# Performance work log

Measured on AMD Instinct MI355X. Metric: run time of the kernel, lower is better.

The kernel has to match this reference:

```python
import jax, jax.numpy as jnp
import numpy as np

D_MODEL = 1024
N_HEADS = 16
D_K = D_MODEL // N_HEADS
B, S = 2, 2048


def setup_inputs() -> dict:
    key = jax.random.key(0)
    ks = jax.random.split(key, 11)
    def lin(kw, kb, fan_in):
        bound = 1.0 / np.sqrt(fan_in)
        W = jax.random.uniform(kw, (fan_in, D_MODEL), jnp.float32, -bound, bound)
        b = jax.random.uniform(kb, (D_MODEL,), jnp.float32, -bound, bound)
        return W, b
    Wq, bq = lin(ks[0], ks[1], D_MODEL)
    Wk, bk = lin(ks[2], ks[3], D_MODEL)
    Wv, bv = lin(ks[4], ks[5], D_MODEL)
    Wo, bo = lin(ks[6], ks[7], D_MODEL)
    q = jax.random.normal(ks[8], (B, S, D_MODEL), jnp.float32)
    k = jax.random.normal(ks[9], (B, S, D_MODEL), jnp.float32)
    v = jax.random.normal(ks[10], (B, S, D_MODEL), jnp.float32)
    return {"q": q, "k": k, "v": v,
            "Wq": Wq, "bq": bq, "Wk": Wk, "bk": bk,
            "Wv": Wv, "bv": bv, "Wo": Wo, "bo": bo}


def reference(q, k, v, Wq, bq, Wk, bk, Wv, bv, Wo, bo):
    Bz, Sq, _ = q.shape
    def split_heads(x):  # [B,S,D] -> [B,H,S,d_k]
        return x.reshape(x.shape[0], x.shape[1], N_HEADS, D_K).transpose(0, 2, 1, 3)
    qh = split_heads(q @ Wq + bq)
    kh = split_heads(k @ Wk + bk)
    vh = split_heads(v @ Wv + bv)
    scores = jnp.einsum("bhqd,bhkd->bhqk", qh, kh) / jnp.sqrt(jnp.float32(D_K))
    attn = jax.nn.softmax(scores, axis=-1)
    out = jnp.einsum("bhqk,bhkd->bhqd", attn, vh)
    out = out.transpose(0, 2, 1, 3).reshape(Bz, Sq, D_MODEL)
    return out @ Wo + bo
```

## Files before the change

### kernel.cpp

```cpp
#include <hip/hip_runtime.h>
#include <hip/hip_bf16.h>
#include <stdint.h>

typedef __bf16 bf16;
typedef __bf16 bf16x8 __attribute__((ext_vector_type(8)));
typedef __bf16 bf16x4 __attribute__((ext_vector_type(4)));
typedef float  f32x4  __attribute__((ext_vector_type(4)));
typedef float  f32x16 __attribute__((ext_vector_type(16)));
typedef uint32_t u32;

#define MFMA16(a,b,c) __builtin_amdgcn_mfma_f32_16x16x32_bf16((a),(b),(c),0,0,0)
#define MFMA32(a,b,c) __builtin_amdgcn_mfma_f32_32x32x16_bf16((a),(b),(c),0,0,0)

#define QSCL 0.1803368801111204f

__device__ __forceinline__ u32 sx32(u32 x) {
    return (u32)__shfl_xor((int)x, 32, 64);
}
__device__ __forceinline__ float swapred_max(float v) {
    return fmaxf(v, __builtin_bit_cast(float, sx32(__builtin_bit_cast(u32, v))));
}
__device__ __forceinline__ float swapred_sum(float v) {
    return v + __builtin_bit_cast(float, sx32(__builtin_bit_cast(u32, v)));
}
__device__ __forceinline__ u32 pkbf(float lo, float hi) {
    union { bf16 h[2]; u32 u; } un;
    un.h[0] = (bf16)lo; un.h[1] = (bf16)hi;
    return un.u;
}
__device__ __forceinline__ void pack_frags(const float* p, int hi, bf16x8& f0, bf16x8& f1) {
    u32 k01 = pkbf(p[0],  p[1]),  k23 = pkbf(p[2],  p[3]);
    u32 k45 = pkbf(p[4],  p[5]),  k67 = pkbf(p[6],  p[7]);
    u32 k89 = pkbf(p[8],  p[9]),  kab = pkbf(p[10], p[11]);
    u32 kcd = pkbf(p[12], p[13]), kef = pkbf(p[14], p[15]);
    u32 x01 = sx32(k01), x23 = sx32(k23), x45 = sx32(k45), x67 = sx32(k67);
    u32 x89 = sx32(k89), xab = sx32(kab), xcd = sx32(kcd), xef = sx32(kef);
    union { u32 w[4]; bf16x8 v; } u0, u1;
    u0.w[0] = hi ? x45 : k01;  u0.w[1] = hi ? x67 : k23;
    u0.w[2] = hi ? k45 : x01;  u0.w[3] = hi ? k67 : x23;
    u1.w[0] = hi ? xcd : k89;  u1.w[1] = hi ? xef : kab;
    u1.w[2] = hi ? kcd : x89;  u1.w[3] = hi ? kef : xab;
    f0 = u0.v; f1 = u1.v;
}

__global__ __launch_bounds__(256) void k_cvt3(const float* __restrict__ a, const float* __restrict__ b,
                                              const float* __restrict__ c,
                                              bf16* __restrict__ x, bf16* __restrict__ y,
                                              bf16* __restrict__ z) {
    int i = blockIdx.x * 256 + threadIdx.x;
    int t = i >> 20;
    int r = (i & 1048575) << 2;
    const float* s = (t == 0) ? a : ((t == 1) ? b : c);
    bf16* d = (t == 0) ? x : ((t == 1) ? y : z);
    float4 v = *(const float4*)&s[r];
    bf16x4 w = {(bf16)v.x, (bf16)v.y, (bf16)v.z, (bf16)v.w};
    *(bf16x4*)&d[r] = w;
}
__global__ __launch_bounds__(256) void k_cvt1(const float* __restrict__ s, bf16* __restrict__ d) {
    int r = (blockIdx.x * 256 + threadIdx.x) << 2;
    float4 v = *(const float4*)&s[r];
    bf16x4 w = {(bf16)v.x, (bf16)v.y, (bf16)v.z, (bf16)v.w};
    *(bf16x4*)&d[r] = w;
}

__global__ __launch_bounds__(256) void k_transpose_w(const float* __restrict__ W,
                                                     bf16* __restrict__ Wt, float scale) {
    __shared__ bf16 t[64][65];
    const int n0 = blockIdx.x * 64, k0 = blockIdx.y * 64;
    for (int i = 0; i < 16; ++i) {
        int idx = threadIdx.x + i * 256, r = idx >> 6, c = idx & 63;
        t[r][c] = (bf16)(W[(size_t)(k0 + r) * 1024 + n0 + c] * scale);
    }
    __syncthreads();
    for (int i = 0; i < 16; ++i) {
        int idx = threadIdx.x + i * 256, r = idx >> 6, c = idx & 63;
        Wt[(size_t)(n0 + r) * 1024 + k0 + c] = t[c][r];
    }
}

__device__ __forceinline__ void gemm_tile(const bf16* __restrict__ A, const bf16* __restrict__ Bt,
                                          const float* __restrict__ bias, float bscale,
                                          void* __restrict__ Cp, int out_mode, int m0, int n0,
                                          bf16 (*As)[64], bf16 (*Bs)[64]) {
    const int tid = threadIdx.x;
    const int wid = tid >> 6, lane = tid & 63, lg = lane >> 4, lm = lane & 15;
    const int wr = wid >> 1, wc = wid & 1;
    const int grow = tid >> 3, gcol = (tid & 7) << 3;

    f32x4 acc[4][4] = {};

    for (int kt = 0; kt < 16; ++kt) {
        const int k0 = kt << 6;
        __syncthreads();
#pragma unroll
        for (int p = 0; p < 4; ++p) {
            __builtin_amdgcn_global_load_lds(
                (const __attribute__((address_space(1))) void*)(A + (size_t)(m0 + p * 32 + grow) * 1024 + k0 + gcol),
                (__attribute__((address_space(3))) void*)(&As[p * 32 + wid * 8][0]), 16, 0, 0);
            __builtin_amdgcn_global_load_lds(
                (const __attribute__((address_space(1))) void*)(Bt + (size_t)(n0 + p * 32 + grow) * 1024 + k0 + gcol),
                (__attribute__((address_space(3))) void*)(&Bs[p * 32 + wid * 8][0]), 16, 0, 0);
        }
        __syncthreads();
#pragma unroll
        for (int kk = 0; kk < 2; ++kk) {
            bf16x8 a[4], b[4];
#pragma unroll
            for (int i = 0; i < 4; ++i) a[i] = *(const bf16x8*)&As[wr * 64 + i * 16 + lm][kk * 32 + lg * 8];
#pragma unroll
            for (int j = 0; j < 4; ++j) b[j] = *(const bf16x8*)&Bs[wc * 64 + j * 16 + lm][kk * 32 + lg * 8];
#pragma unroll
            for (int i = 0; i < 4; ++i)
#pragma unroll
                for (int j = 0; j < 4; ++j) acc[i][j] = MFMA16(a[i], b[j], acc[i][j]);
        }
    }

    for (int i = 0; i < 4; ++i) {
        for (int j = 0; j < 4; ++j) {
            int col = n0 + wc * 64 + j * 16 + lm;
            for (int q = 0; q < 4; ++q) {
                int row = m0 + wr * 64 + i * 16 + lg * 4 + q;
                if (out_mode == 0) {
                    float val = acc[i][j][q] + bscale * bias[col];
                    int bb = row >> 11, s = row & 2047, h = col >> 6, d = col & 63;
                    ((bf16*)Cp)[(((size_t)bb * 16 + h) * 2048 + s) * 64 + d] = (bf16)val;
                } else {
                    float val = acc[i][j][q] + bias[row];
                    size_t idx = (((size_t)(col >> 11) * 16 + (row >> 6)) * 64 + (row & 63)) * 2048 + (col & 2047);
                    ((bf16*)Cp)[idx] = (bf16)val;
                }
            }
        }
    }
}

__device__ __forceinline__ void tile_decode(int r, int& m0, int& n0) {
    int xcd = r & 7, slot = (r >> 3) & 3, n = (r >> 5) & 7;
    m0 = (xcd * 4 + slot) * 128;
    n0 = n * 128;
}
__device__ __forceinline__ void tile_decode_vt(int r, int& m0, int& n0) {
    int xcd = r & 7, loc = r >> 3;
    int nslot = loc & 3, m = loc >> 2;
    n0 = (xcd * 4 + nslot) * 128;
    m0 = m * 128;
}

__global__ __launch_bounds__(256, 4) void k_gemm_proj(const bf16* __restrict__ A,
                                                      const bf16* __restrict__ Bt,
                                                      const float* __restrict__ bias, float bscale,
                                                      void* __restrict__ Cp) {
    __shared__ bf16 As[128][64];
    __shared__ bf16 Bs[128][64];
    int m0, n0;
    tile_decode(blockIdx.x, m0, n0);
    gemm_tile(A, Bt, bias, bscale, Cp, 0, m0, n0, As, Bs);
}

__global__ __launch_bounds__(256, 4) void k_gemm_vt(const bf16* __restrict__ Wtv,
                                                    const bf16* __restrict__ vc,
                                                    const float* __restrict__ bias,
                                                    bf16* __restrict__ Vtb) {
    __shared__ bf16 As[128][64];
    __shared__ bf16 Bs[128][64];
    int m0, n0;
    tile_decode_vt(blockIdx.x, m0, n0);
    gemm_tile(Wtv, vc, bias, 1.0f, (void*)Vtb, 2, m0, n0, As, Bs);
}

__global__ __launch_bounds__(256, 4) void k_gemm_qkv(const bf16* __restrict__ qc, const bf16* __restrict__ kc,
                                                     const bf16* __restrict__ vc,
                                                     const bf16* __restrict__ Wtq, const bf16* __restrict__ Wtk,
                                                     const bf16* __restrict__ Wtv,
                                                     const float* __restrict__ bq, const float* __restrict__ bk,
                                                     const float* __restrict__ bv,
                                                     bf16* __restrict__ Qb, bf16* __restrict__ Kb,
                                                     bf16* __restrict__ Vtb) {
    __shared__ bf16 As[128][64];
    __shared__ bf16 Bs[128][64];
    int l = blockIdx.x, z = l >> 8, r = l & 255;
    int m0, n0;
    if (z == 2) {
        tile_decode_vt(r, m0, n0);
        gemm_tile(Wtv, vc, bv, 1.0f, (void*)Vtb, 2, m0, n0, As, Bs);
    } else {
        tile_decode(r, m0, n0);
        const bf16* A  = (z == 0) ? qc : kc;
        const bf16* Bt = (z == 0) ? Wtq : Wtk;
        const float* bias = (z == 0) ? bq : bk;
        float bscale = (z == 0) ? QSCL : 1.0f;
        bf16* Cp = (z == 0) ? Qb : Kb;
        gemm_tile(A, Bt, bias, bscale, (void*)Cp, 0, m0, n0, As, Bs);
    }
}

__global__ __launch_bounds__(256, 4) void k_gemm_out(const bf16* __restrict__ A,
                                                     const bf16* __restrict__ Bt,
                                                     const float* __restrict__ bias,
                                                     float* __restrict__ C) {
    __shared__ bf16 As[128][64];
    __shared__ bf16 Bs[64][64];
    const int tid = threadIdx.x;
    const int wid = tid >> 6, lane = tid & 63, lg = lane >> 4, lm = lane & 15;
    const int grow = tid >> 3, gcol = (tid & 7) << 3;
    const int r = blockIdx.x;
    const int xcd = r & 7, loc = r >> 3;
    const int mslot = loc & 3, n = loc >> 2;
    const int m0 = (xcd * 4 + mslot) * 128, n0 = n * 64;

    f32x4 acc[2][4] = {};

    for (int kt = 0; kt < 16; ++kt) {
        const int k0 = kt << 6;
        __syncthreads();
#pragma unroll
        for (int p = 0; p < 4; ++p)
            __builtin_amdgcn_global_load_lds(
                (const __attribute__((address_space(1))) void*)(A + (size_t)(m0 + p * 32 + grow) * 1024 + k0 + gcol),
                (__attribute__((address_space(3))) void*)(&As[p * 32 + wid * 8][0]), 16, 0, 0);
#pragma unroll
        for (int p = 0; p < 2; ++p)
            __builtin_amdgcn_global_load_lds(
                (const __attribute__((address_space(1))) void*)(Bt + (size_t)(n0 + p * 32 + grow) * 1024 + k0 + gcol),
                (__attribute__((address_space(3))) void*)(&Bs[p * 32 + wid * 8][0]), 16, 0, 0);
        __syncthreads();
#pragma unroll
        for (int kk = 0; kk < 2; ++kk) {
            bf16x8 a[2], b[4];
#pragma unroll
            for (int i = 0; i < 2; ++i) a[i] = *(const bf16x8*)&As[wid * 32 + i * 16 + lm][kk * 32 + lg * 8];
#pragma unroll
            for (int j = 0; j < 4; ++j) b[j] = *(const bf16x8*)&Bs[j * 16 + lm][kk * 32 + lg * 8];
#pragma unroll
            for (int i = 0; i < 2; ++i)
#pragma unroll
                for (int j = 0; j < 4; ++j) acc[i][j] = MFMA16(a[i], b[j], acc[i][j]);
        }
    }

    for (int i = 0; i < 2; ++i) {
        for (int j = 0; j < 4; ++j) {
            int col = n0 + j * 16 + lm;
            float bv = bias[col];
            for (int q = 0; q < 4; ++q) {
                int row = m0 + wid * 32 + i * 16 + lg * 4 + q;
                C[(size_t)row * 1024 + col] = acc[i][j][q] + bv;
            }
        }
    }
}

__global__ __launch_bounds__(512, 2) void k_attn(const bf16* __restrict__ Q,
                                                 const bf16* __restrict__ Kb,
                                                 const bf16* __restrict__ Vt,
                                                 bf16* __restrict__ Out) {
    __shared__ bf16 Ks[2][64 * 64];
    __shared__ bf16 Vs[2][64 * 64];
    const int tid = threadIdx.x;
    const int wid = tid >> 6, lane = tid & 63;
    const int lm = lane & 31, hi = lane >> 5;
    const int bid = blockIdx.x;
    const int bh = bid & 31, qt = bid >> 5;
    const int bb = bh >> 4, h = bh & 15;
    const int qrow = qt * 256 + wid * 32 + lm;
    const size_t qk_base = (size_t)bh * (2048 * 64);
    const size_t vt_base = (size_t)bh * (64 * 2048);

    const int srow = tid >> 3, sc8 = tid & 7;
    const int cse = (sc8 ^ (srow & 7)) * 8;
    const bf16* kstage = Kb + qk_base + (size_t)srow * 64 + cse;
    const bf16* vstage = Vt + vt_base + (size_t)srow * 2048 + cse;
    const int ldsoff = wid * 1024;

    bf16x8 qf[4];
    {
        const bf16* qp = Q + qk_base + (size_t)qrow * 64 + hi * 8;
#pragma unroll
        for (int f = 0; f < 4; ++f) qf[f] = *(const bf16x8*)(qp + f * 16);
    }

    f32x16 O0 = {}, O1 = {};
    float mrow = -1e30f, lsum = 0.f;

    const int swz = (lm & 7);

    __builtin_amdgcn_global_load_lds(
        (const __attribute__((address_space(1))) void*)(kstage),
        (__attribute__((address_space(3))) void*)((char*)&Ks[0][0] + ldsoff), 16, 0, 0);
    __builtin_amdgcn_global_load_lds(
        (const __attribute__((address_space(1))) void*)(vstage),
        (__attribute__((address_space(3))) void*)((char*)&Vs[0][0] + ldsoff), 16, 0, 0);
    __syncthreads();

    int cur = 0;
#pragma unroll 1
    for (int kt = 0; kt < 32; ++kt) {
        if (kt + 1 < 32) {
            __builtin_amdgcn_global_load_lds(
                (const __attribute__((address_space(1))) void*)(kstage + (size_t)(kt + 1) * 4096),
                (__attribute__((address_space(3))) void*)((char*)&Ks[cur ^ 1][0] + ldsoff), 16, 0, 0);
            __builtin_amdgcn_global_load_lds(
                (const __attribute__((address_space(1))) void*)(vstage + (size_t)(kt + 1) * 64),
                (__attribute__((address_space(3))) void*)((char*)&Vs[cur ^ 1][0] + ldsoff), 16, 0, 0);
        }

        const char* Ksc = (const char*)&Ks[cur][0];
        const char* Vsc = (const char*)&Vs[cur][0];

        bf16x8 kf0[4], kf1[4];
#pragma unroll
        for (int f = 0; f < 4; ++f) {
            int ch = (f << 1) | hi;
            kf0[f] = *(const bf16x8*)(Ksc + lm * 128 + ((ch ^ swz) << 4));
            kf1[f] = *(const bf16x8*)(Ksc + (lm + 32) * 128 + ((ch ^ swz) << 4));
        }
        bf16x8 vf0[4], vf1[4];
#pragma unroll
        for (int ks = 0; ks < 4; ++ks) {
            int ch = (ks << 1) | hi;
            vf0[ks] = *(const bf16x8*)(Vsc + lm * 128 + ((ch ^ swz) << 4));
            vf1[ks] = *(const bf16x8*)(Vsc + (lm + 32) * 128 + ((ch ^ swz) << 4));
        }

        f32x16 s0 = {}, s1 = {};
#pragma unroll
        for (int f = 0; f < 4; ++f) {
            s0 = MFMA32(kf0[f], qf[f], s0);
            s1 = MFMA32(kf1[f], qf[f], s1);
        }

        float pe0[16], pe1[16];
#pragma unroll
        for (int r = 0; r < 16; ++r) pe0[r] = __builtin_amdgcn_exp2f(s0[r] - mrow);
#pragma unroll
        for (int r = 0; r < 16; ++r) pe1[r] = __builtin_amdgcn_exp2f(s1[r] - mrow);

        float t8[8];
#pragma unroll
        for (int r = 0; r < 8; ++r)
            t8[r] = fmaxf(fmaxf(s0[r], s0[r + 8]), fmaxf(s1[r], s1[r + 8]));
#pragma unroll
        for (int st = 4; st; st >>= 1)
#pragma unroll
            for (int r = 0; r < st; ++r) t8[r] = fmaxf(t8[r], t8[r + st]);
        float pm = swapred_max(t8[0]);

        if (!__all(pm <= mrow + 8.0f)) {
            float mnew = fmaxf(mrow, pm);
            float corr = __builtin_amdgcn_exp2f(mrow - mnew);
            lsum *= corr;
            O0 *= corr;
            O1 *= corr;
            mrow = mnew;
#pragma unroll
            for (int r = 0; r < 16; ++r) pe0[r] = __builtin_amdgcn_exp2f(s0[r] - mrow);
#pragma unroll
            for (int r = 0; r < 16; ++r) pe1[r] = __builtin_amdgcn_exp2f(s1[r] - mrow);
        }

        float u8[8];
#pragma unroll
        for (int r = 0; r < 8; ++r) u8[r] = (pe0[r] + pe0[r + 8]) + (pe1[r] + pe1[r + 8]);
#pragma unroll
        for (int st = 4; st; st >>= 1)
#pragma unroll
            for (int r = 0; r < st; ++r) u8[r] = u8[r] + u8[r + st];
        lsum += u8[0];

        bf16x8 pf[4];
        pack_frags(pe0, hi, pf[0], pf[1]);
        pack_frags(pe1, hi, pf[2], pf[3]);

#pragma unroll
        for (int ks = 0; ks < 4; ++ks) {
            O0 = MFMA32(vf0[ks], pf[ks], O0);
            O1 = MFMA32(vf1[ks], pf[ks], O1);
        }

        __syncthreads();
        cur ^= 1;
    }

    float lrow = swapred_sum(lsum);
    float inv = 1.0f / lrow;
    bf16* op = Out + ((size_t)bb * 2048 + qrow) * 1024 + h * 64 + 4 * hi;
#pragma unroll
    for (int t = 0; t < 4; ++t) {
        bf16x4 w0, w1;
#pragma unroll
        for (int e = 0; e < 4; ++e) {
            w0[e] = (bf16)(O0[4 * t + e] * inv);
            w1[e] = (bf16)(O1[4 * t + e] * inv);
        }
        *(bf16x4*)(op + 8 * t)      = w0;
        *(bf16x4*)(op + 32 + 8 * t) = w1;
    }
}

extern "C" void kernel_launch(void* const* d_in, const int* in_sizes, int n_in,
                              void* d_out, int out_size, void* d_ws, size_t ws_size,
                              hipStream_t stream) {
    const float* q  = (const float*)d_in[0];
    const float* k  = (const float*)d_in[1];
    const float* v  = (const float*)d_in[2];
    const float* Wq = (const float*)d_in[3];
    const float* bq = (const float*)d_in[4];
    const float* Wk = (const float*)d_in[5];
    const float* bk = (const float*)d_in[6];
    const float* Wv = (const float*)d_in[7];
    const float* bv = (const float*)d_in[8];
    const float* Wo = (const float*)d_in[9];
    const float* bo = (const float*)d_in[10];

    char* ws = (char*)d_ws;
    const size_t MB = 1ull << 20;
    const dim3 twg(16, 16), blk(256);

    if (ws_size >= 64 * MB) {
        bf16* Wtq = (bf16*)(ws + 0 * MB);
        bf16* Wtk = (bf16*)(ws + 2 * MB);
        bf16* Wtv = (bf16*)(ws + 4 * MB);
        bf16* Wto = (bf16*)(ws + 6 * MB);
        bf16* qc  = (bf16*)(ws + 8 * MB);
        bf16* kc  = (bf16*)(ws + 16 * MB);
        bf16* vc  = (bf16*)(ws + 24 * MB);
        bf16* Qb  = (bf16*)(ws + 32 * MB);
        bf16* Kb  = (bf16*)(ws + 40 * MB);
        bf16* Vtb = (bf16*)(ws + 48 * MB);
        bf16* AOb = kc;

        k_transpose_w<<<twg, blk, 0, stream>>>(Wq, Wtq, QSCL);
        k_transpose_w<<<twg, blk, 0, stream>>>(Wk, Wtk, 1.0f);
        k_transpose_w<<<twg, blk, 0, stream>>>(Wv, Wtv, 1.0f);
        k_transpose_w<<<twg, blk, 0, stream>>>(Wo, Wto, 1.0f);
        k_cvt3<<<12288, blk, 0, stream>>>(q, k, v, qc, kc, vc);
        k_gemm_qkv<<<768, blk, 0, stream>>>(qc, kc, vc, Wtq, Wtk, Wtv, bq, bk, bv, Qb, Kb, Vtb);
        k_attn<<<256, 512, 0, stream>>>(Qb, Kb, Vtb, AOb);
        k_gemm_out<<<512, blk, 0, stream>>>(AOb, Wto, bo, (float*)d_out);
    } else {
        bf16* Wt   = (bf16*)(ws + 0 * MB);
        bf16* Qb   = (bf16*)(ws + 2 * MB);
        bf16* Kb   = (bf16*)(ws + 10 * MB);
        bf16* Vtb  = (bf16*)(ws + 18 * MB);
        bf16* AOb  = (bf16*)(ws + 26 * MB);
        bf16* Cb   = (bf16*)d_out;

        k_cvt1<<<4096, blk, 0, stream>>>(q, Cb);
        k_transpose_w<<<twg, blk, 0, stream>>>(Wq, Wt, QSCL);
        k_gemm_proj<<<256, blk, 0, stream>>>(Cb, Wt, bq, QSCL, (void*)Qb);
        k_cvt1<<<4096, blk, 0, stream>>>(k, Cb);
        k_transpose_w<<<twg, blk, 0, stream>>>(Wk, Wt, 1.0f);
        k_gemm_proj<<<256, blk, 0, stream>>>(Cb, Wt, bk, 1.0f, (void*)Kb);
        k_cvt1<<<4096, blk, 0, stream>>>(v, Cb);
        k_transpose_w<<<twg, blk, 0, stream>>>(Wv, Wt, 1.0f);
        k_gemm_vt<<<256, blk, 0, stream>>>(Wt, Cb, bv, Vtb);
        k_transpose_w<<<twg, blk, 0, stream>>>(Wo, Wt, 1.0f);
        k_attn<<<256, 512, 0, stream>>>(Qb, Kb, Vtb, AOb);
        k_gemm_out<<<512, blk, 0, stream>>>(AOb, Wt, bo, (float*)d_out);
    }
}
```

Measured before the change: 144.2 us.

## Split attention over KV halves with a combine pass; merge weight transposes

The attention kernel now splits the key/value sequence into two halves per block, and each wave handles 64 query rows (two 32-row groups) against 32-key tiles. Unnormalized partial outputs go to a bf16 scratch buffer, with row max and sum stored separately. A new combine kernel merges the two partials into the head-interleaved layout. The four weight-transpose launches also become one launch over a z grid dimension. The aim is to reuse each K/V LDS tile for more query rows and cut launch overhead, at the cost of an extra kernel pass and extra global traffic for the partials.

```diff
diff --git a/kernel.cpp b/kernel.cpp
--- a/kernel.cpp
+++ b/kernel.cpp
@@ -63,10 +63,9 @@
     *(bf16x4*)&d[r] = w;
 }
 
-__global__ __launch_bounds__(256) void k_transpose_w(const float* __restrict__ W,
-                                                     bf16* __restrict__ Wt, float scale) {
+__device__ __forceinline__ void transpose_body(const float* __restrict__ W, bf16* __restrict__ Wt,
+                                               float scale, int n0, int k0) {
     __shared__ bf16 t[64][65];
-    const int n0 = blockIdx.x * 64, k0 = blockIdx.y * 64;
     for (int i = 0; i < 16; ++i) {
         int idx = threadIdx.x + i * 256, r = idx >> 6, c = idx & 63;
         t[r][c] = (bf16)(W[(size_t)(k0 + r) * 1024 + n0 + c] * scale);
@@ -76,6 +75,19 @@
         int idx = threadIdx.x + i * 256, r = idx >> 6, c = idx & 63;
         Wt[(size_t)(n0 + r) * 1024 + k0 + c] = t[c][r];
     }
+}
+__global__ __launch_bounds__(256) void k_transpose_w(const float* __restrict__ W,
+                                                     bf16* __restrict__ Wt, float scale) {
+    transpose_body(W, Wt, scale, blockIdx.x * 64, blockIdx.y * 64);
+}
+__global__ __launch_bounds__(256) void k_transpose_w4(const float* __restrict__ Wq, const float* __restrict__ Wk,
+                                                      const float* __restrict__ Wv, const float* __restrict__ Wo,
+                                                      bf16* __restrict__ Wtq, bf16* __restrict__ Wtk,
+                                                      bf16* __restrict__ Wtv, bf16* __restrict__ Wto) {
+    int z = blockIdx.z;
+    const float* W = (z == 0) ? Wq : (z == 1) ? Wk : (z == 2) ? Wv : Wo;
+    bf16* Wt = (z == 0) ? Wtq : (z == 1) ? Wtk : (z == 2) ? Wtv : Wto;
+    transpose_body(W, Wt, (z == 0) ? QSCL : 1.0f, blockIdx.x * 64, blockIdx.y * 64);
 }
 
 __device__ __forceinline__ void gemm_tile(const bf16* __restrict__ A, const bf16* __restrict__ Bt,
@@ -254,148 +266,187 @@
 __global__ __launch_bounds__(512, 2) void k_attn(const bf16* __restrict__ Q,
                                                  const bf16* __restrict__ Kb,
                                                  const bf16* __restrict__ Vt,
-                                                 bf16* __restrict__ Out) {
-    __shared__ bf16 Ks[2][64 * 64];
-    __shared__ bf16 Vs[2][64 * 64];
+                                                 bf16* __restrict__ Opart,
+                                                 float* __restrict__ ml) {
+    __shared__ bf16 Ks[2][32 * 64];
+    __shared__ bf16 Vs[2][32 * 64];
     const int tid = threadIdx.x;
     const int wid = tid >> 6, lane = tid & 63;
     const int lm = lane & 31, hi = lane >> 5;
     const int bid = blockIdx.x;
-    const int bh = bid & 31, qt = bid >> 5;
-    const int bb = bh >> 4, h = bh & 15;
-    const int qrow = qt * 256 + wid * 32 + lm;
+    const int bh = bid & 31, qt = (bid >> 5) & 3, sp = bid >> 7;
     const size_t qk_base = (size_t)bh * (2048 * 64);
     const size_t vt_base = (size_t)bh * (64 * 2048);
-
-    const int srow = tid >> 3, sc8 = tid & 7;
-    const int cse = (sc8 ^ (srow & 7)) * 8;
-    const bf16* kstage = Kb + qk_base + (size_t)srow * 64 + cse;
-    const bf16* vstage = Vt + vt_base + (size_t)srow * 2048 + cse;
-    const int ldsoff = wid * 1024;
-
-    bf16x8 qf[4];
+    const int kt0 = sp * 32, kt1 = kt0 + 32;
+    const int qrowA = qt * 512 + wid * 64 + lm;
+    const int qrowB = qrowA + 32;
+
+    const int u = tid & 255;
+    const int srow = u >> 3, pc = u & 7;
+    const int lc = pc ^ (srow & 7);
+    const bf16* kst = Kb + qk_base + (size_t)srow * 64 + lc * 8;
+    const bf16* vst = Vt + vt_base + (size_t)(srow + ((lc >> 2) << 5)) * 2048 + (lc & 3) * 8;
+    const int sbase = (wid & 3) * 1024;
+
+#define STAGE(T, BUF)                                                                             \
+    do {                                                                                          \
+        if (tid < 256)                                                                            \
+            __builtin_amdgcn_global_load_lds(                                                     \
+                (const __attribute__((address_space(1))) void*)(kst + (size_t)(T) * 2048),        \
+                (__attribute__((address_space(3))) void*)((char*)&Ks[BUF][0] + sbase), 16, 0, 0); \
+        else                                                                                      \
+            __builtin_amdgcn_global_load_lds(                                                     \
+                (const __attribute__((address_space(1))) void*)(vst + (size_t)(T) * 32),          \
+                (__attribute__((address_space(3))) void*)((char*)&Vs[BUF][0] + sbase), 16, 0, 0); \
+    } while (0)
+
+    bf16x8 qfA[4], qfB[4];
     {
-        const bf16* qp = Q + qk_base + (size_t)qrow * 64 + hi * 8;
-#pragma unroll
-        for (int f = 0; f < 4; ++f) qf[f] = *(const bf16x8*)(qp + f * 16);
-    }
-
-    f32x16 O0 = {}, O1 = {};
-    float mrow = -1e30f, lsum = 0.f;
-
-    const int swz = (lm & 7);
-
-    __builtin_amdgcn_global_load_lds(
-        (const __attribute__((address_space(1))) void*)(kstage),
-        (__attribute__((address_space(3))) void*)((char*)&Ks[0][0] + ldsoff), 16, 0, 0);
-    __builtin_amdgcn_global_load_lds(
-        (const __attribute__((address_space(1))) void*)(vstage),
-        (__attribute__((address_space(3))) void*)((char*)&Vs[0][0] + ldsoff), 16, 0, 0);
+        const bf16* qpA = Q + qk_base + (size_t)qrowA * 64 + hi * 8;
+        const bf16* qpB = qpA + 32 * 64;
+#pragma unroll
+        for (int f = 0; f < 4; ++f) {
+            qfA[f] = *(const bf16x8*)(qpA + f * 16);
+            qfB[f] = *(const bf16x8*)(qpB + f * 16);
+        }
+    }
+
+    f32x16 O0A = {}, O1A = {}, O0B = {}, O1B = {};
+    float mA = -1e30f, mB = -1e30f, lsA = 0.f, lsB = 0.f;
+    const int swz = lm & 7;
+
+    STAGE(kt0, 0);
     __syncthreads();
 
     int cur = 0;
 #pragma unroll 1
-    for (int kt = 0; kt < 32; ++kt) {
-        if (kt + 1 < 32) {
-            __builtin_amdgcn_global_load_lds(
-                (const __attribute__((address_space(1))) void*)(kstage + (size_t)(kt + 1) * 4096),
-                (__attribute__((address_space(3))) void*)((char*)&Ks[cur ^ 1][0] + ldsoff), 16, 0, 0);
-            __builtin_amdgcn_global_load_lds(
-                (const __attribute__((address_space(1))) void*)(vstage + (size_t)(kt + 1) * 64),
-                (__attribute__((address_space(3))) void*)((char*)&Vs[cur ^ 1][0] + ldsoff), 16, 0, 0);
-        }
+    for (int kt = kt0; kt < kt1; ++kt) {
+        if (kt + 1 < kt1) STAGE(kt + 1, cur ^ 1);
 
         const char* Ksc = (const char*)&Ks[cur][0];
         const char* Vsc = (const char*)&Vs[cur][0];
 
-        bf16x8 kf0[4], kf1[4];
-#pragma unroll
-        for (int f = 0; f < 4; ++f) {
-            int ch = (f << 1) | hi;
-            kf0[f] = *(const bf16x8*)(Ksc + lm * 128 + ((ch ^ swz) << 4));
-            kf1[f] = *(const bf16x8*)(Ksc + (lm + 32) * 128 + ((ch ^ swz) << 4));
-        }
-        bf16x8 vf0[4], vf1[4];
-#pragma unroll
-        for (int ks = 0; ks < 4; ++ks) {
-            int ch = (ks << 1) | hi;
-            vf0[ks] = *(const bf16x8*)(Vsc + lm * 128 + ((ch ^ swz) << 4));
-            vf1[ks] = *(const bf16x8*)(Vsc + (lm + 32) * 128 + ((ch ^ swz) << 4));
-        }
-
-        f32x16 s0 = {}, s1 = {};
-#pragma unroll
-        for (int f = 0; f < 4; ++f) {
-            s0 = MFMA32(kf0[f], qf[f], s0);
-            s1 = MFMA32(kf1[f], qf[f], s1);
-        }
-
-        float pe0[16], pe1[16];
-#pragma unroll
-        for (int r = 0; r < 16; ++r) pe0[r] = __builtin_amdgcn_exp2f(s0[r] - mrow);
-#pragma unroll
-        for (int r = 0; r < 16; ++r) pe1[r] = __builtin_amdgcn_exp2f(s1[r] - mrow);
-
-        float t8[8];
-#pragma unroll
-        for (int r = 0; r < 8; ++r)
-            t8[r] = fmaxf(fmaxf(s0[r], s0[r + 8]), fmaxf(s1[r], s1[r + 8]));
+        bf16x8 kf[4];
+#pragma unroll
+        for (int f = 0; f < 4; ++f)
+            kf[f] = *(const bf16x8*)(Ksc + lm * 128 + (((((f << 1) | hi)) ^ swz) << 4));
+
+        f32x16 sA = {}, sB = {};
+#pragma unroll
+        for (int f = 0; f < 4; ++f) sA = MFMA32(kf[f], qfA[f], sA);
+#pragma unroll
+        for (int f = 0; f < 4; ++f) sB = MFMA32(kf[f], qfB[f], sB);
+
+        float tA[8], tB[8];
+#pragma unroll
+        for (int r = 0; r < 8; ++r) { tA[r] = fmaxf(sA[r], sA[r + 8]); tB[r] = fmaxf(sB[r], sB[r + 8]); }
 #pragma unroll
         for (int st = 4; st; st >>= 1)
 #pragma unroll
-            for (int r = 0; r < st; ++r) t8[r] = fmaxf(t8[r], t8[r + st]);
-        float pm = swapred_max(t8[0]);
-
-        if (!__all(pm <= mrow + 8.0f)) {
-            float mnew = fmaxf(mrow, pm);
-            float corr = __builtin_amdgcn_exp2f(mrow - mnew);
-            lsum *= corr;
-            O0 *= corr;
-            O1 *= corr;
-            mrow = mnew;
-#pragma unroll
-            for (int r = 0; r < 16; ++r) pe0[r] = __builtin_amdgcn_exp2f(s0[r] - mrow);
-#pragma unroll
-            for (int r = 0; r < 16; ++r) pe1[r] = __builtin_amdgcn_exp2f(s1[r] - mrow);
-        }
-
-        float u8[8];
-#pragma unroll
-        for (int r = 0; r < 8; ++r) u8[r] = (pe0[r] + pe0[r + 8]) + (pe1[r] + pe1[r + 8]);
+            for (int r = 0; r < st; ++r) { tA[r] = fmaxf(tA[r], tA[r + st]); tB[r] = fmaxf(tB[r], tB[r + st]); }
+        float pmA = swapred_max(tA[0]);
+        float pmB = swapred_max(tB[0]);
+
+        if (!__all(pmA <= mA + 8.0f)) {
+            float mn = fmaxf(mA, pmA);
+            float c = __builtin_amdgcn_exp2f(mA - mn);
+            lsA *= c; O0A *= c; O1A *= c; mA = mn;
+        }
+        if (!__all(pmB <= mB + 8.0f)) {
+            float mn = fmaxf(mB, pmB);
+            float c = __builtin_amdgcn_exp2f(mB - mn);
+            lsB *= c; O0B *= c; O1B *= c; mB = mn;
+        }
+
+        float peA[16], peB[16];
+#pragma unroll
+        for (int r = 0; r < 16; ++r) peA[r] = __builtin_amdgcn_exp2f(sA[r] - mA);
+#pragma unroll
+        for (int r = 0; r < 16; ++r) peB[r] = __builtin_amdgcn_exp2f(sB[r] - mB);
+        float uA[8], uB[8];
+#pragma unroll
+        for (int r = 0; r < 8; ++r) { uA[r] = peA[r] + peA[r + 8]; uB[r] = peB[r] + peB[r + 8]; }
 #pragma unroll
         for (int st = 4; st; st >>= 1)
 #pragma unroll
-            for (int r = 0; r < st; ++r) u8[r] = u8[r] + u8[r + st];
-        lsum += u8[0];
-
-        bf16x8 pf[4];
-        pack_frags(pe0, hi, pf[0], pf[1]);
-        pack_frags(pe1, hi, pf[2], pf[3]);
-
-#pragma unroll
-        for (int ks = 0; ks < 4; ++ks) {
-            O0 = MFMA32(vf0[ks], pf[ks], O0);
-            O1 = MFMA32(vf1[ks], pf[ks], O1);
-        }
+            for (int r = 0; r < st; ++r) { uA[r] += uA[r + st]; uB[r] += uB[r + st]; }
+        lsA += uA[0];
+        lsB += uB[0];
+
+        bf16x8 pfA[2], pfB[2];
+        pack_frags(peA, hi, pfA[0], pfA[1]);
+        pack_frags(peB, hi, pfB[0], pfB[1]);
+
+        bf16x8 vf[2][2];
+#pragma unroll
+        for (int dh = 0; dh < 2; ++dh)
+#pragma unroll
+            for (int ks = 0; ks < 2; ++ks)
+                vf[dh][ks] = *(const bf16x8*)(Vsc + lm * 128 + ((((dh << 2) | (ks << 1) | hi) ^ swz) << 4));
+
+        O0A = MFMA32(vf[0][0], pfA[0], O0A);
+        O0A = MFMA32(vf[0][1], pfA[1], O0A);
+        O1A = MFMA32(vf[1][0], pfA[0], O1A);
+        O1A = MFMA32(vf[1][1], pfA[1], O1A);
+        O0B = MFMA32(vf[0][0], pfB[0], O0B);
+        O0B = MFMA32(vf[0][1], pfB[1], O0B);
+        O1B = MFMA32(vf[1][0], pfB[0], O1B);
+        O1B = MFMA32(vf[1][1], pfB[1], O1B);
 
         __syncthreads();
         cur ^= 1;
     }
-
-    float lrow = swapred_sum(lsum);
-    float inv = 1.0f / lrow;
-    bf16* op = Out + ((size_t)bb * 2048 + qrow) * 1024 + h * 64 + 4 * hi;
+#undef STAGE
+
+    float lrA = swapred_sum(lsA);
+    float lrB = swapred_sum(lsB);
+    const size_t r2A = ((size_t)bh * 2048 + qrowA) * 2 + sp;
+    const size_t r2B = r2A + 64;
+    bf16* opA = Opart + r2A * 64 + 4 * hi;
+    bf16* opB = Opart + r2B * 64 + 4 * hi;
 #pragma unroll
     for (int t = 0; t < 4; ++t) {
-        bf16x4 w0, w1;
+        bf16x4 a0, a1, b0, b1;
 #pragma unroll
         for (int e = 0; e < 4; ++e) {
-            w0[e] = (bf16)(O0[4 * t + e] * inv);
-            w1[e] = (bf16)(O1[4 * t + e] * inv);
-        }
-        *(bf16x4*)(op + 8 * t)      = w0;
-        *(bf16x4*)(op + 32 + 8 * t) = w1;
-    }
+            a0[e] = (bf16)O0A[4 * t + e];
+            a1[e] = (bf16)O1A[4 * t + e];
+            b0[e] = (bf16)O0B[4 * t + e];
+            b1[e] = (bf16)O1B[4 * t + e];
+        }
+        *(bf16x4*)(opA + 8 * t)      = a0;
+        *(bf16x4*)(opA + 32 + 8 * t) = a1;
+        *(bf16x4*)(opB + 8 * t)      = b0;
+        *(bf16x4*)(opB + 32 + 8 * t) = b1;
+    }
+    if (hi == 0) {
+        float2 vA = {mA, lrA};
+        float2 vB = {mB, lrB};
+        ((float2*)ml)[r2A] = vA;
+        ((float2*)ml)[r2B] = vB;
+    }
+}
+
+__global__ __launch_bounds__(256) void k_combine(const bf16* __restrict__ Opart,
+                                                 const float* __restrict__ ml,
+                                                 bf16* __restrict__ AOb) {
+    int e8 = blockIdx.x * 256 + threadIdx.x;
+    int row = e8 >> 3, dc = (e8 & 7) << 3;
+    float2 ml0 = ((const float2*)ml)[row * 2 + 0];
+    float2 ml1 = ((const float2*)ml)[row * 2 + 1];
+    float M  = fmaxf(ml0.x, ml1.x);
+    float w0 = __builtin_amdgcn_exp2f(ml0.x - M);
+    float w1 = __builtin_amdgcn_exp2f(ml1.x - M);
+    float L  = w0 * ml0.y + w1 * ml1.y;
+    float a0 = w0 / L, a1 = w1 / L;
+    bf16x8 p0 = *(const bf16x8*)&Opart[((size_t)row * 2 + 0) * 64 + dc];
+    bf16x8 p1 = *(const bf16x8*)&Opart[((size_t)row * 2 + 1) * 64 + dc];
+    bf16x8 o;
+#pragma unroll
+    for (int j = 0; j < 8; ++j) o[j] = (bf16)(a0 * (float)p0[j] + a1 * (float)p1[j]);
+    int bh = row >> 11, qrow = row & 2047;
+    int bb = bh >> 4, h = bh & 15;
+    *(bf16x8*)&AOb[((size_t)bb * 2048 + qrow) * 1024 + h * 64 + dc] = o;
 }
 
 extern "C" void kernel_launch(void* const* d_in, const int* in_sizes, int n_in,
@@ -416,6 +467,7 @@
     char* ws = (char*)d_ws;
     const size_t MB = 1ull << 20;
     const dim3 twg(16, 16), blk(256);
+    bf16* Opart = (bf16*)d_out;
 
     if (ws_size >= 64 * MB) {
         bf16* Wtq = (bf16*)(ws + 0 * MB);
@@ -428,23 +480,23 @@
         bf16* Qb  = (bf16*)(ws + 32 * MB);
         bf16* Kb  = (bf16*)(ws + 40 * MB);
         bf16* Vtb = (bf16*)(ws + 48 * MB);
-        bf16* AOb = kc;
-
-        k_transpose_w<<<twg, blk, 0, stream>>>(Wq, Wtq, QSCL);
-        k_transpose_w<<<twg, blk, 0, stream>>>(Wk, Wtk, 1.0f);
-        k_transpose_w<<<twg, blk, 0, stream>>>(Wv, Wtv, 1.0f);
-        k_transpose_w<<<twg, blk, 0, stream>>>(Wo, Wto, 1.0f);
+        float* mlb = (float*)qc;
+        bf16* AOb  = kc;
+
+        k_transpose_w4<<<dim3(16, 16, 4), blk, 0, stream>>>(Wq, Wk, Wv, Wo, Wtq, Wtk, Wtv, Wto);
         k_cvt3<<<12288, blk, 0, stream>>>(q, k, v, qc, kc, vc);
         k_gemm_qkv<<<768, blk, 0, stream>>>(qc, kc, vc, Wtq, Wtk, Wtv, bq, bk, bv, Qb, Kb, Vtb);
-        k_attn<<<256, 512, 0, stream>>>(Qb, Kb, Vtb, AOb);
+        k_attn<<<256, 512, 0, stream>>>(Qb, Kb, Vtb, Opart, mlb);
+        k_combine<<<2048, blk, 0, stream>>>(Opart, mlb, AOb);
         k_gemm_out<<<512, blk, 0, stream>>>(AOb, Wto, bo, (float*)d_out);
     } else {
         bf16* Wt   = (bf16*)(ws + 0 * MB);
         bf16* Qb   = (bf16*)(ws + 2 * MB);
         bf16* Kb   = (bf16*)(ws + 10 * MB);
         bf16* Vtb  = (bf16*)(ws + 18 * MB);
-        bf16* AOb  = (bf16*)(ws + 26 * MB);
+        float* mlb = (float*)(ws + 26 * MB);
         bf16* Cb   = (bf16*)d_out;
+        bf16* AOb  = Qb;
 
         k_cvt1<<<4096, blk, 0, stream>>>(q, Cb);
         k_transpose_w<<<twg, blk, 0, stream>>>(Wq, Wt, QSCL);
@@ -456,7 +508,8 @@
         k_transpose_w<<<twg, blk, 0, stream>>>(Wv, Wt, 1.0f);
         k_gemm_vt<<<256, blk, 0, stream>>>(Wt, Cb, bv, Vtb);
         k_transpose_w<<<twg, blk, 0, stream>>>(Wo, Wt, 1.0f);
-        k_attn<<<256, 512, 0, stream>>>(Qb, Kb, Vtb, AOb);
+        k_attn<<<256, 512, 0, stream>>>(Qb, Kb, Vtb, Opart, mlb);
+        k_combine<<<2048, blk, 0, stream>>>(Opart, mlb, AOb);
         k_gemm_out<<<512, blk, 0, stream>>>(AOb, Wt, bo, (float*)d_out);
     }
 }
```

Result: no change. 142.5 us (-1.2%).

## Fuse fp32-to-bf16 input conversion into GEMM tile loads and batch weight transposes

Applied to the files above, without the earlier changes.

The separate conversion kernel that cast q, k and v from fp32 to bf16 is removed. The projection GEMMs now read the fp32 activations directly, convert them in registers and store them to LDS. This drops a full write and re-read of the bf16 copies and one kernel launch. The four weight-transpose launches are also merged into a single launch using a z grid dimension. In exchange, fp32 tiles go through registers instead of the async global-to-LDS path, so each tile load moves twice the bytes and may overlap less with compute.

```diff
diff --git a/kernel.cpp b/kernel.cpp
--- a/kernel.cpp
+++ b/kernel.cpp
@@ -43,30 +43,9 @@
     f0 = u0.v; f1 = u1.v;
 }
 
-__global__ __launch_bounds__(256) void k_cvt3(const float* __restrict__ a, const float* __restrict__ b,
-                                              const float* __restrict__ c,
-                                              bf16* __restrict__ x, bf16* __restrict__ y,
-                                              bf16* __restrict__ z) {
-    int i = blockIdx.x * 256 + threadIdx.x;
-    int t = i >> 20;
-    int r = (i & 1048575) << 2;
-    const float* s = (t == 0) ? a : ((t == 1) ? b : c);
-    bf16* d = (t == 0) ? x : ((t == 1) ? y : z);
-    float4 v = *(const float4*)&s[r];
-    bf16x4 w = {(bf16)v.x, (bf16)v.y, (bf16)v.z, (bf16)v.w};
-    *(bf16x4*)&d[r] = w;
-}
-__global__ __launch_bounds__(256) void k_cvt1(const float* __restrict__ s, bf16* __restrict__ d) {
-    int r = (blockIdx.x * 256 + threadIdx.x) << 2;
-    float4 v = *(const float4*)&s[r];
-    bf16x4 w = {(bf16)v.x, (bf16)v.y, (bf16)v.z, (bf16)v.w};
-    *(bf16x4*)&d[r] = w;
-}
-
-__global__ __launch_bounds__(256) void k_transpose_w(const float* __restrict__ W,
-                                                     bf16* __restrict__ Wt, float scale) {
+__device__ __forceinline__ void transpose_body(const float* __restrict__ W, bf16* __restrict__ Wt,
+                                               float scale, int n0, int k0) {
     __shared__ bf16 t[64][65];
-    const int n0 = blockIdx.x * 64, k0 = blockIdx.y * 64;
     for (int i = 0; i < 16; ++i) {
         int idx = threadIdx.x + i * 256, r = idx >> 6, c = idx & 63;
         t[r][c] = (bf16)(W[(size_t)(k0 + r) * 1024 + n0 + c] * scale);
@@ -77,11 +56,25 @@
         Wt[(size_t)(n0 + r) * 1024 + k0 + c] = t[c][r];
     }
 }
-
-__device__ __forceinline__ void gemm_tile(const bf16* __restrict__ A, const bf16* __restrict__ Bt,
-                                          const float* __restrict__ bias, float bscale,
-                                          void* __restrict__ Cp, int out_mode, int m0, int n0,
-                                          bf16 (*As)[64], bf16 (*Bs)[64]) {
+__global__ __launch_bounds__(256) void k_transpose_w(const float* __restrict__ W,
+                                                     bf16* __restrict__ Wt, float scale) {
+    transpose_body(W, Wt, scale, blockIdx.x * 64, blockIdx.y * 64);
+}
+__global__ __launch_bounds__(256) void k_transpose_w4(const float* __restrict__ Wq, const float* __restrict__ Wk,
+                                                      const float* __restrict__ Wv, const float* __restrict__ Wo,
+                                                      bf16* __restrict__ Wtq, bf16* __restrict__ Wtk,
+                                                      bf16* __restrict__ Wtv, bf16* __restrict__ Wto) {
+    int z = blockIdx.z;
+    const float* W = (z == 0) ? Wq : (z == 1) ? Wk : (z == 2) ? Wv : Wo;
+    bf16* Wt = (z == 0) ? Wtq : (z == 1) ? Wtk : (z == 2) ? Wtv : Wto;
+    transpose_body(W, Wt, (z == 0) ? QSCL : 1.0f, blockIdx.x * 64, blockIdx.y * 64);
+}
+
+template <int A_F32, int B_F32>
+__device__ __forceinline__ void gemm_tile2(const void* __restrict__ Ap, const void* __restrict__ Btp,
+                                           const float* __restrict__ bias, float bscale,
+                                           void* __restrict__ Cp, int out_mode, int m0, int n0,
+                                           bf16 (*As)[64], bf16 (*Bs)[64]) {
     const int tid = threadIdx.x;
     const int wid = tid >> 6, lane = tid & 63, lg = lane >> 4, lm = lane & 15;
     const int wr = wid >> 1, wc = wid & 1;
@@ -94,12 +87,35 @@
         __syncthreads();
 #pragma unroll
         for (int p = 0; p < 4; ++p) {
-            __builtin_amdgcn_global_load_lds(
-                (const __attribute__((address_space(1))) void*)(A + (size_t)(m0 + p * 32 + grow) * 1024 + k0 + gcol),
-                (__attribute__((address_space(3))) void*)(&As[p * 32 + wid * 8][0]), 16, 0, 0);
-            __builtin_amdgcn_global_load_lds(
-                (const __attribute__((address_space(1))) void*)(Bt + (size_t)(n0 + p * 32 + grow) * 1024 + k0 + gcol),
-                (__attribute__((address_space(3))) void*)(&Bs[p * 32 + wid * 8][0]), 16, 0, 0);
+            const int r = p * 32 + grow;
+            if constexpr (A_F32) {
+                const float* A = (const float*)Ap;
+                const float* src = A + (size_t)(m0 + r) * 1024 + k0 + gcol;
+                float4 v0 = *(const float4*)src;
+                float4 v1 = *(const float4*)(src + 4);
+                bf16x8 w = {(bf16)v0.x, (bf16)v0.y, (bf16)v0.z, (bf16)v0.w,
+                            (bf16)v1.x, (bf16)v1.y, (bf16)v1.z, (bf16)v1.w};
+                *(bf16x8*)&As[r][gcol] = w;
+            } else {
+                const bf16* A = (const bf16*)Ap;
+                __builtin_amdgcn_global_load_lds(
+                    (const __attribute__((address_space(1))) void*)(A + (size_t)(m0 + r) * 1024 + k0 + gcol),
+                    (__attribute__((address_space(3))) void*)(&As[p * 32 + wid * 8][0]), 16, 0, 0);
+            }
+            if constexpr (B_F32) {
+                const float* B = (const float*)Btp;
+                const float* src = B + (size_t)(n0 + r) * 1024 + k0 + gcol;
+                float4 v0 = *(const float4*)src;
+                float4 v1 = *(const float4*)(src + 4);
+                bf16x8 w = {(bf16)v0.x, (bf16)v0.y, (bf16)v0.z, (bf16)v0.w,
+                            (bf16)v1.x, (bf16)v1.y, (bf16)v1.z, (bf16)v1.w};
+                *(bf16x8*)&Bs[r][gcol] = w;
+            } else {
+                const bf16* Bt = (const bf16*)Btp;
+                __builtin_amdgcn_global_load_lds(
+                    (const __attribute__((address_space(1))) void*)(Bt + (size_t)(n0 + r) * 1024 + k0 + gcol),
+                    (__attribute__((address_space(3))) void*)(&Bs[p * 32 + wid * 8][0]), 16, 0, 0);
+            }
         }
         __syncthreads();
 #pragma unroll
@@ -147,7 +163,7 @@
     m0 = m * 128;
 }
 
-__global__ __launch_bounds__(256, 4) void k_gemm_proj(const bf16* __restrict__ A,
+__global__ __launch_bounds__(256, 4) void k_gemm_proj(const float* __restrict__ A,
                                                       const bf16* __restrict__ Bt,
                                                       const float* __restrict__ bias, float bscale,
                                                       void* __restrict__ Cp) {
@@ -155,22 +171,22 @@
     __shared__ bf16 Bs[128][64];
     int m0, n0;
     tile_decode(blockIdx.x, m0, n0);
-    gemm_tile(A, Bt, bias, bscale, Cp, 0, m0, n0, As, Bs);
+    gemm_tile2<1, 0>((const void*)A, (const void*)Bt, bias, bscale, Cp, 0, m0, n0, As, Bs);
 }
 
 __global__ __launch_bounds__(256, 4) void k_gemm_vt(const bf16* __restrict__ Wtv,
-                                                    const bf16* __restrict__ vc,
+                                                    const float* __restrict__ v,
                                                     const float* __restrict__ bias,
                                                     bf16* __restrict__ Vtb) {
     __shared__ bf16 As[128][64];
     __shared__ bf16 Bs[128][64];
     int m0, n0;
     tile_decode_vt(blockIdx.x, m0, n0);
-    gemm_tile(Wtv, vc, bias, 1.0f, (void*)Vtb, 2, m0, n0, As, Bs);
-}
-
-__global__ __launch_bounds__(256, 4) void k_gemm_qkv(const bf16* __restrict__ qc, const bf16* __restrict__ kc,
-                                                     const bf16* __restrict__ vc,
+    gemm_tile2<0, 1>((const void*)Wtv, (const void*)v, bias, 1.0f, (void*)Vtb, 2, m0, n0, As, Bs);
+}
+
+__global__ __launch_bounds__(256, 4) void k_gemm_qkv(const float* __restrict__ q, const float* __restrict__ k,
+                                                     const float* __restrict__ v,
                                                      const bf16* __restrict__ Wtq, const bf16* __restrict__ Wtk,
                                                      const bf16* __restrict__ Wtv,
                                                      const float* __restrict__ bq, const float* __restrict__ bk,
@@ -183,15 +199,15 @@
     int m0, n0;
     if (z == 2) {
         tile_decode_vt(r, m0, n0);
-        gemm_tile(Wtv, vc, bv, 1.0f, (void*)Vtb, 2, m0, n0, As, Bs);
+        gemm_tile2<0, 1>((const void*)Wtv, (const void*)v, bv, 1.0f, (void*)Vtb, 2, m0, n0, As, Bs);
     } else {
         tile_decode(r, m0, n0);
-        const bf16* A  = (z == 0) ? qc : kc;
-        const bf16* Bt = (z == 0) ? Wtq : Wtk;
+        const float* A  = (z == 0) ? q : k;
+        const bf16* Bt  = (z == 0) ? Wtq : Wtk;
         const float* bias = (z == 0) ? bq : bk;
         float bscale = (z == 0) ? QSCL : 1.0f;
         bf16* Cp = (z == 0) ? Qb : Kb;
-        gemm_tile(A, Bt, bias, bscale, (void*)Cp, 0, m0, n0, As, Bs);
+        gemm_tile2<1, 0>((const void*)A, (const void*)Bt, bias, bscale, (void*)Cp, 0, m0, n0, As, Bs);
     }
 }
 
@@ -417,25 +433,18 @@
     const size_t MB = 1ull << 20;
     const dim3 twg(16, 16), blk(256);
 
-    if (ws_size >= 64 * MB) {
+    if (ws_size >= 40 * MB) {
         bf16* Wtq = (bf16*)(ws + 0 * MB);
         bf16* Wtk = (bf16*)(ws + 2 * MB);
         bf16* Wtv = (bf16*)(ws + 4 * MB);
         bf16* Wto = (bf16*)(ws + 6 * MB);
-        bf16* qc  = (bf16*)(ws + 8 * MB);
-        bf16* kc  = (bf16*)(ws + 16 * MB);
-        bf16* vc  = (bf16*)(ws + 24 * MB);
-        bf16* Qb  = (bf16*)(ws + 32 * MB);
-        bf16* Kb  = (bf16*)(ws + 40 * MB);
-        bf16* Vtb = (bf16*)(ws + 48 * MB);
-        bf16* AOb = kc;
-
-        k_transpose_w<<<twg, blk, 0, stream>>>(Wq, Wtq, QSCL);
-        k_transpose_w<<<twg, blk, 0, stream>>>(Wk, Wtk, 1.0f);
-        k_transpose_w<<<twg, blk, 0, stream>>>(Wv, Wtv, 1.0f);
-        k_transpose_w<<<twg, blk, 0, stream>>>(Wo, Wto, 1.0f);
-        k_cvt3<<<12288, blk, 0, stream>>>(q, k, v, qc, kc, vc);
-        k_gemm_qkv<<<768, blk, 0, stream>>>(qc, kc, vc, Wtq, Wtk, Wtv, bq, bk, bv, Qb, Kb, Vtb);
+        bf16* Qb  = (bf16*)(ws + 8 * MB);
+        bf16* Kb  = (bf16*)(ws + 16 * MB);
+        bf16* Vtb = (bf16*)(ws + 24 * MB);
+        bf16* AOb = (bf16*)(ws + 32 * MB);
+
+        k_transpose_w4<<<dim3(16, 16, 4), blk, 0, stream>>>(Wq, Wk, Wv, Wo, Wtq, Wtk, Wtv, Wto);
+        k_gemm_qkv<<<768, blk, 0, stream>>>(q, k, v, Wtq, Wtk, Wtv, bq, bk, bv, Qb, Kb, Vtb);
         k_attn<<<256, 512, 0, stream>>>(Qb, Kb, Vtb, AOb);
         k_gemm_out<<<512, blk, 0, stream>>>(AOb, Wto, bo, (float*)d_out);
     } else {
@@ -444,17 +453,13 @@
         bf16* Kb   = (bf16*)(ws + 10 * MB);
         bf16* Vtb  = (bf16*)(ws + 18 * MB);
         bf16* AOb  = (bf16*)(ws + 26 * MB);
-        bf16* Cb   = (bf16*)d_out;
-
-        k_cvt1<<<4096, blk, 0, stream>>>(q, Cb);
+
         k_transpose_w<<<twg, blk, 0, stream>>>(Wq, Wt, QSCL);
-        k_gemm_proj<<<256, blk, 0, stream>>>(Cb, Wt, bq, QSCL, (void*)Qb);
-        k_cvt1<<<4096, blk, 0, stream>>>(k, Cb);
+        k_gemm_proj<<<256, blk, 0, stream>>>(q, Wt, bq, QSCL, (void*)Qb);
         k_transpose_w<<<twg, blk, 0, stream>>>(Wk, Wt, 1.0f);
-        k_gemm_proj<<<256, blk, 0, stream>>>(Cb, Wt, bk, 1.0f, (void*)Kb);
-        k_cvt1<<<4096, blk, 0, stream>>>(v, Cb);
+        k_gemm_proj<<<256, blk, 0, stream>>>(k, Wt, bk, 1.0f, (void*)Kb);
         k_transpose_w<<<twg, blk, 0, stream>>>(Wv, Wt, 1.0f);
-        k_gemm_vt<<<256, blk, 0, stream>>>(Wt, Cb, bv, Vtb);
+        k_gemm_vt<<<256, blk, 0, stream>>>(Wt, v, bv, Vtb);
         k_transpose_w<<<twg, blk, 0, stream>>>(Wo, Wt, 1.0f);
         k_attn<<<256, 512, 0, stream>>>(Qb, Kb, Vtb, AOb);
         k_gemm_out<<<512, blk, 0, stream>>>(AOb, Wt, bo, (float*)d_out);
```

After: 136.8 us, median of 2. -5.1%, faster.
